# Kernel optimization log

Hardware: AMD Instinct MI355X
Metric: run time of the kernel (lower is better)

## Reference

```python
import jax, jax.numpy as jnp
import numpy as np

N = 50000
E = 800000
NHID = 128
NOUT = 64
NLAYER = 4
BN_EPS = 1e-5


def setup_inputs() -> dict:
    key = jax.random.key(0)
    ks = jax.random.split(key, 4)
    x = jax.random.normal(ks[0], (N, NHID), dtype=jnp.float32)
    edge_index = jax.random.randint(ks[1], (2, E), 0, N, dtype=jnp.int32)
    Ws = jax.random.normal(ks[2], (NLAYER, NHID, NHID), dtype=jnp.float32) / np.sqrt(NHID)
    bs = jnp.zeros((NLAYER, NHID), dtype=jnp.float32)
    gammas = jnp.ones((NLAYER, NHID), dtype=jnp.float32)
    betas = jnp.zeros((NLAYER, NHID), dtype=jnp.float32)
    Wout = jax.random.normal(ks[3], (NHID, NOUT), dtype=jnp.float32) / np.sqrt(NHID)
    bout = jnp.zeros((NOUT,), dtype=jnp.float32)
    return {"x": x, "edge_index": edge_index, "Ws": Ws, "bs": bs,
            "gammas": gammas, "betas": betas, "Wout": Wout, "bout": bout}


def _gcn_conv(x, src, dst, norm, W, b):
    # GCNConv: h = x W, then symmetric-normalized scatter-add over edges (+ self loops already in src/dst)
    h = x @ W                                   # [N, nhid]
    msgs = h[src] * norm[:, None]               # [E+N, nhid] gather + scale
    agg = jax.ops.segment_sum(msgs, dst, num_segments=N)  # scatter-add
    return agg + b


def _batchnorm(x, gamma, beta):
    mean = jnp.mean(x, axis=0)
    var = jnp.mean(jnp.square(x - mean), axis=0)  # biased var (torch BN)
    return (x - mean) * jax.lax.rsqrt(var + BN_EPS) * gamma + beta


def reference(x, edge_index, Ws, bs, gammas, betas, Wout, bout):
    # add self loops
    loops = jnp.arange(N, dtype=edge_index.dtype)
    src = jnp.concatenate([edge_index[0], loops])
    dst = jnp.concatenate([edge_index[1], loops])
    # symmetric degree normalization: deg^-1/2[src] * deg^-1/2[dst]
    deg = jax.ops.segment_sum(jnp.ones_like(dst, dtype=x.dtype), dst, num_segments=N)
    dinv = jax.lax.rsqrt(jnp.maximum(deg, 1.0))
    norm = dinv[src] * dinv[dst]

    prev = x
    for l in range(NLAYER):
        h = _gcn_conv(x, src, dst, norm, Ws[l], bs[l])
        h = _batchnorm(h, gammas[l], betas[l])
        h = jax.nn.relu(h)
        # dropout p=0.0 -> identity
        x = h + prev  # residual
        prev = x
    return x @ Wout + bout
```

## Files before the change

### kernel.cpp

```cpp
#include <hip/hip_runtime.h>

#define NN 50000
#define NE 800000
#define NH 128
#define NO 64
#define NL 4
#define BN_EPS 1e-5f
#define NB1 ((NN + 255) / 256)

typedef __attribute__((ext_vector_type(8))) short short8;
typedef __attribute__((ext_vector_type(4))) float f32x4;

__device__ inline unsigned short f2bf(float f) {
    unsigned int u = __float_as_uint(f);
    return (unsigned short)((u + 0x7fffu + ((u >> 16) & 1u)) >> 16);
}
__device__ inline float bflo(unsigned int u) { return __uint_as_float(u << 16); }
__device__ inline float bfhi(unsigned int u) { return __uint_as_float(u & 0xffff0000u); }
__device__ inline unsigned pk(float a, float b) {
    return (unsigned)f2bf(a) | ((unsigned)f2bf(b) << 16);
}

__global__ void k_degrank(const int* __restrict__ dst, int* __restrict__ deg,
                          int* __restrict__ rank) {
    int e = blockIdx.x * 256 + threadIdx.x;
    if (e < NE) rank[e] = atomicAdd(&deg[dst[e]], 1);
}

__global__ void k_dinv(const int* __restrict__ deg, float* __restrict__ dinv) {
    int i = blockIdx.x * 256 + threadIdx.x;
    if (i < NN) dinv[i] = rsqrtf((float)deg[i] + 1.0f);
}

__global__ void k_scan1(const int* __restrict__ deg, int* __restrict__ off, int* __restrict__ aux) {
    __shared__ int ls[256];
    int i = blockIdx.x * 256 + threadIdx.x;
    int v = (i < NN) ? deg[i] : 0;
    ls[threadIdx.x] = v;
    __syncthreads();
    for (int s = 1; s < 256; s <<= 1) {
        int t = (threadIdx.x >= s) ? ls[threadIdx.x - s] : 0;
        __syncthreads();
        ls[threadIdx.x] += t;
        __syncthreads();
    }
    if (i < NN) off[i] = ls[threadIdx.x] - v;
    if (threadIdx.x == 255) aux[blockIdx.x] = ls[255];
}

__global__ void k_scan2(int* __restrict__ aux) {
    __shared__ int ls[256];
    int v = (threadIdx.x < NB1) ? aux[threadIdx.x] : 0;
    ls[threadIdx.x] = v;
    __syncthreads();
    for (int s = 1; s < 256; s <<= 1) {
        int t = (threadIdx.x >= s) ? ls[threadIdx.x - s] : 0;
        __syncthreads();
        ls[threadIdx.x] += t;
        __syncthreads();
    }
    if (threadIdx.x < NB1) aux[threadIdx.x] = ls[threadIdx.x] - v;
}

__global__ void k_scan3(int* __restrict__ off, const int* __restrict__ aux) {
    int i = blockIdx.x * 256 + threadIdx.x;
    if (i < NN) off[i] += aux[blockIdx.x];
}

__global__ void k_fill(const int* __restrict__ src, const int* __restrict__ dst,
                       const int* __restrict__ off, const int* __restrict__ rank,
                       int* __restrict__ csr) {
    int e = blockIdx.x * 256 + threadIdx.x;
    if (e < NE) csr[off[dst[e]] + rank[e]] = src[e];
}

__global__ void k_packW(const float* __restrict__ Ws, unsigned short* __restrict__ Wpk) {
    int t = blockIdx.x * 256 + threadIdx.x;
    if (t >= NL * 16384) return;
    int l = t >> 14, r = t & 16383;
    int ks = r >> 12, ct = (r >> 9) & 7, lane = (r >> 3) & 63, i = r & 7;
    int k = ks * 32 + (lane >> 4) * 8 + i;
    int n = ct * 16 + (lane & 15);
    Wpk[t] = f2bf(Ws[l * 16384 + k * 128 + n]);
}

__global__ void k_packWout(const float* __restrict__ Wout, unsigned short* __restrict__ Wpk) {
    int r = blockIdx.x * 256 + threadIdx.x;
    if (r >= 8192) return;
    int ks = r >> 11, ct = (r >> 9) & 3, lane = (r >> 3) & 63, i = r & 7;
    int k = ks * 32 + (lane >> 4) * 8 + i;
    int n = ct * 16 + (lane & 15);
    Wpk[r] = f2bf(Wout[k * 64 + n]);
}

__global__ __launch_bounds__(256) void k_fg0(const float* __restrict__ X,
                                             const unsigned short* __restrict__ Wpk,
                                             const float* __restrict__ dinv,
                                             unsigned short* __restrict__ Hd) {
    int w = threadIdx.x >> 6, l = threadIdx.x & 63;
    int row0 = blockIdx.x * 64 + w * 16;
    int lo = l & 15, hi = l >> 4;
    int arow = row0 + lo;
    int crow = (arow < NN) ? arow : NN - 1;
    short8 frag[4];
#pragma unroll
    for (int g = 0; g < 4; g++) {
        int cs = g * 32 + hi * 8;
        float4 p0 = *(const float4*)&X[(size_t)crow * NH + cs];
        float4 p1 = *(const float4*)&X[(size_t)crow * NH + cs + 4];
        short8 f;
        f[0] = (short)f2bf(p0.x); f[1] = (short)f2bf(p0.y);
        f[2] = (short)f2bf(p0.z); f[3] = (short)f2bf(p0.w);
        f[4] = (short)f2bf(p1.x); f[5] = (short)f2bf(p1.y);
        f[6] = (short)f2bf(p1.z); f[7] = (short)f2bf(p1.w);
        frag[g] = f;
    }
    const short8* Wv = (const short8*)Wpk;
    int srow = row0 + hi * 4;
    float dv[4];
#pragma unroll
    for (int r = 0; r < 4; r++) dv[r] = (srow + r < NN) ? dinv[srow + r] : 0.0f;
#pragma unroll
    for (int ct = 0; ct < 8; ct++) {
        f32x4 acc = {0.0f, 0.0f, 0.0f, 0.0f};
#pragma unroll
        for (int g = 0; g < 4; g++)
            acc = __builtin_amdgcn_mfma_f32_16x16x32_bf16(frag[g], Wv[(g * 8 + ct) * 64 + l], acc, 0, 0, 0);
        int col = ct * 16 + lo;
#pragma unroll
        for (int r = 0; r < 4; r++) {
            int grow = srow + r;
            if (grow < NN) Hd[grow * NH + col] = f2bf(acc[r] * dv[r]);
        }
    }
}

__global__ __launch_bounds__(256) void k_fg(const unsigned short* __restrict__ AGGb,
                                            const float* __restrict__ scale,
                                            const float* __restrict__ shift,
                                            const float* __restrict__ Xprev,
                                            float* __restrict__ Xout,
                                            const unsigned short* __restrict__ Wpk,
                                            const float* __restrict__ dinv,
                                            unsigned short* __restrict__ Hd) {
    int w = threadIdx.x >> 6, l = threadIdx.x & 63;
    int row0 = blockIdx.x * 64 + w * 16;
    int lo = l & 15, hi = l >> 4;
    int arow = row0 + lo;
    bool valid = arow < NN;
    int crow = valid ? arow : NN - 1;
    short8 frag[4];
#pragma unroll
    for (int g = 0; g < 4; g++) {
        int cs = g * 32 + hi * 8;
        uint4 ab = *(const uint4*)&AGGb[(size_t)crow * NH + cs];
        float4 p0 = *(const float4*)&Xprev[(size_t)crow * NH + cs];
        float4 p1 = *(const float4*)&Xprev[(size_t)crow * NH + cs + 4];
        float4 sc0 = *(const float4*)&scale[cs];
        float4 sc1 = *(const float4*)&scale[cs + 4];
        float4 sh0 = *(const float4*)&shift[cs];
        float4 sh1 = *(const float4*)&shift[cs + 4];
        float o0 = fmaxf(fmaf(bflo(ab.x), sc0.x, sh0.x), 0.0f) + p0.x;
        float o1 = fmaxf(fmaf(bfhi(ab.x), sc0.y, sh0.y), 0.0f) + p0.y;
        float o2 = fmaxf(fmaf(bflo(ab.y), sc0.z, sh0.z), 0.0f) + p0.z;
        float o3 = fmaxf(fmaf(bfhi(ab.y), sc0.w, sh0.w), 0.0f) + p0.w;
        float o4 = fmaxf(fmaf(bflo(ab.z), sc1.x, sh1.x), 0.0f) + p1.x;
        float o5 = fmaxf(fmaf(bfhi(ab.z), sc1.y, sh1.y), 0.0f) + p1.y;
        float o6 = fmaxf(fmaf(bflo(ab.w), sc1.z, sh1.z), 0.0f) + p1.z;
        float o7 = fmaxf(fmaf(bfhi(ab.w), sc1.w, sh1.w), 0.0f) + p1.w;
        if (valid) {
            float4 s0 = {o0, o1, o2, o3}, s1 = {o4, o5, o6, o7};
            *(float4*)&Xout[(size_t)arow * NH + cs] = s0;
            *(float4*)&Xout[(size_t)arow * NH + cs + 4] = s1;
        }
        short8 f;
        f[0] = (short)f2bf(o0); f[1] = (short)f2bf(o1);
        f[2] = (short)f2bf(o2); f[3] = (short)f2bf(o3);
        f[4] = (short)f2bf(o4); f[5] = (short)f2bf(o5);
        f[6] = (short)f2bf(o6); f[7] = (short)f2bf(o7);
        frag[g] = f;
    }
    const short8* Wv = (const short8*)Wpk;
    int srow = row0 + hi * 4;
    float dv[4];
#pragma unroll
    for (int r = 0; r < 4; r++) dv[r] = (srow + r < NN) ? dinv[srow + r] : 0.0f;
#pragma unroll
    for (int ct = 0; ct < 8; ct++) {
        f32x4 acc = {0.0f, 0.0f, 0.0f, 0.0f};
#pragma unroll
        for (int g = 0; g < 4; g++)
            acc = __builtin_amdgcn_mfma_f32_16x16x32_bf16(frag[g], Wv[(g * 8 + ct) * 64 + l], acc, 0, 0, 0);
        int col = ct * 16 + lo;
#pragma unroll
        for (int r = 0; r < 4; r++) {
            int grow = srow + r;
            if (grow < NN) Hd[grow * NH + col] = f2bf(acc[r] * dv[r]);
        }
    }
}

__global__ __launch_bounds__(256) void k_fgout(const unsigned short* __restrict__ AGGb,
                                               const float* __restrict__ scale,
                                               const float* __restrict__ shift,
                                               const float* __restrict__ Xprev,
                                               const unsigned short* __restrict__ Wpk,
                                               const float* __restrict__ b,
                                               float* __restrict__ out) {
    int w = threadIdx.x >> 6, l = threadIdx.x & 63;
    int row0 = blockIdx.x * 64 + w * 16;
    int lo = l & 15, hi = l >> 4;
    int arow = row0 + lo;
    int crow = (arow < NN) ? arow : NN - 1;
    short8 frag[4];
#pragma unroll
    for (int g = 0; g < 4; g++) {
        int cs = g * 32 + hi * 8;
        uint4 ab = *(const uint4*)&AGGb[(size_t)crow * NH + cs];
        float4 p0 = *(const float4*)&Xprev[(size_t)crow * NH + cs];
        float4 p1 = *(const float4*)&Xprev[(size_t)crow * NH + cs + 4];
        float4 sc0 = *(const float4*)&scale[cs];
        float4 sc1 = *(const float4*)&scale[cs + 4];
        float4 sh0 = *(const float4*)&shift[cs];
        float4 sh1 = *(const float4*)&shift[cs + 4];
        short8 f;
        f[0] = (short)f2bf(fmaxf(fmaf(bflo(ab.x), sc0.x, sh0.x), 0.0f) + p0.x);
        f[1] = (short)f2bf(fmaxf(fmaf(bfhi(ab.x), sc0.y, sh0.y), 0.0f) + p0.y);
        f[2] = (short)f2bf(fmaxf(fmaf(bflo(ab.y), sc0.z, sh0.z), 0.0f) + p0.z);
        f[3] = (short)f2bf(fmaxf(fmaf(bfhi(ab.y), sc0.w, sh0.w), 0.0f) + p0.w);
        f[4] = (short)f2bf(fmaxf(fmaf(bflo(ab.z), sc1.x, sh1.x), 0.0f) + p1.x);
        f[5] = (short)f2bf(fmaxf(fmaf(bfhi(ab.z), sc1.y, sh1.y), 0.0f) + p1.y);
        f[6] = (short)f2bf(fmaxf(fmaf(bflo(ab.w), sc1.z, sh1.z), 0.0f) + p1.z);
        f[7] = (short)f2bf(fmaxf(fmaf(bfhi(ab.w), sc1.w, sh1.w), 0.0f) + p1.w);
        frag[g] = f;
    }
    const short8* Wv = (const short8*)Wpk;
    int srow = row0 + hi * 4;
#pragma unroll
    for (int ct = 0; ct < 4; ct++) {
        f32x4 acc = {0.0f, 0.0f, 0.0f, 0.0f};
#pragma unroll
        for (int g = 0; g < 4; g++)
            acc = __builtin_amdgcn_mfma_f32_16x16x32_bf16(frag[g], Wv[(g * 4 + ct) * 64 + l], acc, 0, 0, 0);
        int col = ct * 16 + lo;
        float bb = b[col];
#pragma unroll
        for (int r = 0; r < 4; r++) {
            int grow = srow + r;
            if (grow < NN) out[grow * NO + col] = acc[r] + bb;
        }
    }
}

__global__ __launch_bounds__(256) void k_gather(const unsigned short* __restrict__ Hd,
                                                const int* __restrict__ csr,
                                                const int* __restrict__ off,
                                                const int* __restrict__ deg,
                                                const float* __restrict__ dinv,
                                                unsigned short* __restrict__ AGGb) {
    int g = blockIdx.x * 16 + (threadIdx.x >> 4);
    if (g >= NN) return;
    int q = threadIdx.x & 15;
    const uint4* Hv = (const uint4*)Hd;
    int o = off[g], d = deg[g];
    uint4 h = Hv[g * 16 + q];
    float a0 = bflo(h.x), a1 = bfhi(h.x);
    float a2 = bflo(h.y), a3 = bfhi(h.y);
    float a4 = bflo(h.z), a5 = bfhi(h.z);
    float a6 = bflo(h.w), a7 = bfhi(h.w);
    int j = 0;
    for (; j + 2 <= d; j += 2) {
        int s0 = csr[o + j], s1 = csr[o + j + 1];
        uint4 h0 = Hv[s0 * 16 + q];
        uint4 h1 = Hv[s1 * 16 + q];
        a0 += bflo(h0.x) + bflo(h1.x); a1 += bfhi(h0.x) + bfhi(h1.x);
        a2 += bflo(h0.y) + bflo(h1.y); a3 += bfhi(h0.y) + bfhi(h1.y);
        a4 += bflo(h0.z) + bflo(h1.z); a5 += bfhi(h0.z) + bfhi(h1.z);
        a6 += bflo(h0.w) + bflo(h1.w); a7 += bfhi(h0.w) + bfhi(h1.w);
    }
    if (j < d) {
        int s0 = csr[o + j];
        uint4 h0 = Hv[s0 * 16 + q];
        a0 += bflo(h0.x); a1 += bfhi(h0.x);
        a2 += bflo(h0.y); a3 += bfhi(h0.y);
        a4 += bflo(h0.z); a5 += bfhi(h0.z);
        a6 += bflo(h0.w); a7 += bfhi(h0.w);
    }
    float dv = dinv[g];
    uint4 u;
    u.x = pk(a0 * dv, a1 * dv);
    u.y = pk(a2 * dv, a3 * dv);
    u.z = pk(a4 * dv, a5 * dv);
    u.w = pk(a6 * dv, a7 * dv);
    ((uint4*)AGGb)[g * 16 + q] = u;
}

__global__ __launch_bounds__(256) void k_bn_stats(const unsigned short* __restrict__ AGGb,
                                                  float* __restrict__ sums,
                                                  float* __restrict__ sumsq) {
    int tid = threadIdx.x;
    int col = tid & 127;
    float s = 0.0f, s2 = 0.0f;
    for (int r = blockIdx.x * 2 + (tid >> 7); r < NN; r += gridDim.x * 2) {
        float v = bflo((unsigned)AGGb[(size_t)r * NH + col]);
        s += v;
        s2 = fmaf(v, v, s2);
    }
    __shared__ float ls[256], ls2[256];
    ls[tid] = s; ls2[tid] = s2;
    __syncthreads();
    if (tid < 128) {
        atomicAdd(&sums[col], ls[tid] + ls[tid + 128]);
        atomicAdd(&sumsq[col], ls2[tid] + ls2[tid + 128]);
    }
}

__global__ void k_bn_fin(const float* __restrict__ sums, const float* __restrict__ sumsq,
                         const float* __restrict__ gamma, const float* __restrict__ beta,
                         float* __restrict__ scale, float* __restrict__ shift) {
    int c = threadIdx.x;
    if (c < NH) {
        float mean = sums[c] * (1.0f / NN);
        float var = sumsq[c] * (1.0f / NN) - mean * mean;
        float istd = rsqrtf(var + BN_EPS);
        float sc = istd * gamma[c];
        scale[c] = sc;
        shift[c] = beta[c] - mean * sc;
    }
}

extern "C" void kernel_launch(void* const* d_in, const int* in_sizes, int n_in,
                              void* d_out, int out_size, void* d_ws, size_t ws_size,
                              hipStream_t stream) {
    const float* x    = (const float*)d_in[0];
    const int*   ei   = (const int*)d_in[1];
    const float* Ws   = (const float*)d_in[2];
    const float* gam  = (const float*)d_in[4];
    const float* bet  = (const float*)d_in[5];
    const float* Wout = (const float*)d_in[6];
    const float* bout = (const float*)d_in[7];
    float* out = (float*)d_out;

    const int* src = ei;
    const int* dst = ei + NE;

    char* p = (char*)d_ws;
    auto alloc = [&](size_t bytes) { char* r = p; p += (bytes + 255) & ~(size_t)255; return r; };
    int*   deg_i = (int*)alloc(NN * 4);
    int*   off   = (int*)alloc(NN * 4);
    int*   rank  = (int*)alloc((size_t)NE * 4);
    int*   aux   = (int*)alloc(256 * 4);
    int*   csr   = (int*)alloc((size_t)NE * 4);
    float* dinv  = (float*)alloc(NN * 4);
    float* XA    = (float*)alloc((size_t)NN * NH * 4);
    float* XB    = (float*)alloc((size_t)NN * NH * 4);
    unsigned short* Hd   = (unsigned short*)alloc((size_t)NN * NH * 2);
    unsigned short* AGGb = (unsigned short*)alloc((size_t)NN * NH * 2);
    unsigned short* Wpk  = (unsigned short*)alloc((size_t)NL * NH * NH * 2);
    unsigned short* Wopk = (unsigned short*)alloc((size_t)NH * NO * 2);
    float* sums  = (float*)alloc(NH * 4);
    float* sumsq = (float*)alloc(NH * 4);
    float* scale = (float*)alloc(NH * 4);
    float* shift = (float*)alloc(NH * 4);

    hipMemsetAsync(deg_i, 0, NN * 4, stream);
    k_degrank<<<(NE + 255) / 256, 256, 0, stream>>>(dst, deg_i, rank);
    k_dinv<<<(NN + 255) / 256, 256, 0, stream>>>(deg_i, dinv);
    k_scan1<<<NB1, 256, 0, stream>>>(deg_i, off, aux);
    k_scan2<<<1, 256, 0, stream>>>(aux);
    k_scan3<<<NB1, 256, 0, stream>>>(off, aux);
    k_fill<<<(NE + 255) / 256, 256, 0, stream>>>(src, dst, off, rank, csr);
    k_packW<<<(NL * 16384 + 255) / 256, 256, 0, stream>>>(Ws, Wpk);
    k_packWout<<<32, 256, 0, stream>>>(Wout, Wopk);

    const int GB = (NN + 63) / 64;

    k_fg0<<<GB, 256, 0, stream>>>(x, Wpk, dinv, Hd);

    const float* xprev = x;
    for (int l = 0; l < NL; l++) {
        k_gather<<<(NN + 15) / 16, 256, 0, stream>>>(Hd, csr, off, deg_i, dinv, AGGb);
        hipMemsetAsync(sums, 0, 2 * NH * sizeof(float), stream);
        k_bn_stats<<<512, 256, 0, stream>>>(AGGb, sums, sumsq);
        k_bn_fin<<<1, 128, 0, stream>>>(sums, sumsq, gam + l * NH, bet + l * NH, scale, shift);
        if (l < NL - 1) {
            float* Xout = (l & 1) ? XB : XA;
            k_fg<<<GB, 256, 0, stream>>>(AGGb, scale, shift, xprev, Xout,
                                         Wpk + (size_t)(l + 1) * 16384, dinv, Hd);
            xprev = Xout;
        } else {
            k_fgout<<<GB, 256, 0, stream>>>(AGGb, scale, shift, xprev, Wopk, bout, out);
        }
    }
}
```

Measured before the change: 394.1 us.

## Merge setup kernels, vectorize CSR build, unroll gather, and widen BN stats loads

Measured after the change: 385.8 us. 1.02x faster.

```diff
diff --git a/kernel.cpp b/kernel.cpp
--- a/kernel.cpp
+++ b/kernel.cpp
@@ -23,16 +23,19 @@
 
 __global__ void k_degrank(const int* __restrict__ dst, int* __restrict__ deg,
                           int* __restrict__ rank) {
-    int e = blockIdx.x * 256 + threadIdx.x;
-    if (e < NE) rank[e] = atomicAdd(&deg[dst[e]], 1);
-}
-
-__global__ void k_dinv(const int* __restrict__ deg, float* __restrict__ dinv) {
-    int i = blockIdx.x * 256 + threadIdx.x;
-    if (i < NN) dinv[i] = rsqrtf((float)deg[i] + 1.0f);
-}
-
-__global__ void k_scan1(const int* __restrict__ deg, int* __restrict__ off, int* __restrict__ aux) {
+    int base = (blockIdx.x * 256 + threadIdx.x) * 4;
+    if (base >= NE) return;
+    int4 d4 = *(const int4*)&dst[base];
+    int4 r4;
+    r4.x = atomicAdd(&deg[d4.x], 1);
+    r4.y = atomicAdd(&deg[d4.y], 1);
+    r4.z = atomicAdd(&deg[d4.z], 1);
+    r4.w = atomicAdd(&deg[d4.w], 1);
+    *(int4*)&rank[base] = r4;
+}
+
+__global__ void k_scan1(const int* __restrict__ deg, int* __restrict__ off,
+                        int* __restrict__ aux, float* __restrict__ dinv) {
     __shared__ int ls[256];
     int i = blockIdx.x * 256 + threadIdx.x;
     int v = (i < NN) ? deg[i] : 0;
@@ -44,7 +47,10 @@
         ls[threadIdx.x] += t;
         __syncthreads();
     }
-    if (i < NN) off[i] = ls[threadIdx.x] - v;
+    if (i < NN) {
+        off[i] = ls[threadIdx.x] - v;
+        dinv[i] = rsqrtf((float)v + 1.0f);
+    }
     if (threadIdx.x == 255) aux[blockIdx.x] = ls[255];
 }
 
@@ -70,27 +76,34 @@
 __global__ void k_fill(const int* __restrict__ src, const int* __restrict__ dst,
                        const int* __restrict__ off, const int* __restrict__ rank,
                        int* __restrict__ csr) {
-    int e = blockIdx.x * 256 + threadIdx.x;
-    if (e < NE) csr[off[dst[e]] + rank[e]] = src[e];
-}
-
-__global__ void k_packW(const float* __restrict__ Ws, unsigned short* __restrict__ Wpk) {
+    int base = (blockIdx.x * 256 + threadIdx.x) * 4;
+    if (base >= NE) return;
+    int4 d4 = *(const int4*)&dst[base];
+    int4 r4 = *(const int4*)&rank[base];
+    int4 s4 = *(const int4*)&src[base];
+    int o0 = off[d4.x], o1 = off[d4.y], o2 = off[d4.z], o3 = off[d4.w];
+    csr[o0 + r4.x] = s4.x;
+    csr[o1 + r4.y] = s4.y;
+    csr[o2 + r4.z] = s4.z;
+    csr[o3 + r4.w] = s4.w;
+}
+
+__global__ void k_pack(const float* __restrict__ Ws, const float* __restrict__ Wout,
+                       unsigned short* __restrict__ Wpk, unsigned short* __restrict__ Wopk) {
     int t = blockIdx.x * 256 + threadIdx.x;
-    if (t >= NL * 16384) return;
-    int l = t >> 14, r = t & 16383;
-    int ks = r >> 12, ct = (r >> 9) & 7, lane = (r >> 3) & 63, i = r & 7;
-    int k = ks * 32 + (lane >> 4) * 8 + i;
-    int n = ct * 16 + (lane & 15);
-    Wpk[t] = f2bf(Ws[l * 16384 + k * 128 + n]);
-}
-
-__global__ void k_packWout(const float* __restrict__ Wout, unsigned short* __restrict__ Wpk) {
-    int r = blockIdx.x * 256 + threadIdx.x;
-    if (r >= 8192) return;
-    int ks = r >> 11, ct = (r >> 9) & 3, lane = (r >> 3) & 63, i = r & 7;
-    int k = ks * 32 + (lane >> 4) * 8 + i;
-    int n = ct * 16 + (lane & 15);
-    Wpk[r] = f2bf(Wout[k * 64 + n]);
+    if (t < NL * 16384) {
+        int l = t >> 14, r = t & 16383;
+        int ks = r >> 12, ct = (r >> 9) & 7, lane = (r >> 3) & 63, i = r & 7;
+        int k = ks * 32 + (lane >> 4) * 8 + i;
+        int n = ct * 16 + (lane & 15);
+        Wpk[t] = f2bf(Ws[l * 16384 + k * 128 + n]);
+    } else if (t < NL * 16384 + 8192) {
+        int r = t - NL * 16384;
+        int ks = r >> 11, ct = (r >> 9) & 3, lane = (r >> 3) & 63, i = r & 7;
+        int k = ks * 32 + (lane >> 4) * 8 + i;
+        int n = ct * 16 + (lane & 15);
+        Wopk[r] = f2bf(Wout[k * 64 + n]);
+    }
 }
 
 __global__ __launch_bounds__(256) void k_fg0(const float* __restrict__ X,
@@ -269,16 +282,23 @@
     float a4 = bflo(h.z), a5 = bfhi(h.z);
     float a6 = bflo(h.w), a7 = bfhi(h.w);
     int j = 0;
-    for (; j + 2 <= d; j += 2) {
+    for (; j + 4 <= d; j += 4) {
         int s0 = csr[o + j], s1 = csr[o + j + 1];
+        int s2 = csr[o + j + 2], s3 = csr[o + j + 3];
         uint4 h0 = Hv[s0 * 16 + q];
         uint4 h1 = Hv[s1 * 16 + q];
-        a0 += bflo(h0.x) + bflo(h1.x); a1 += bfhi(h0.x) + bfhi(h1.x);
-        a2 += bflo(h0.y) + bflo(h1.y); a3 += bfhi(h0.y) + bfhi(h1.y);
-        a4 += bflo(h0.z) + bflo(h1.z); a5 += bfhi(h0.z) + bfhi(h1.z);
-        a6 += bflo(h0.w) + bflo(h1.w); a7 += bfhi(h0.w) + bfhi(h1.w);
-    }
-    if (j < d) {
+        uint4 h2 = Hv[s2 * 16 + q];
+        uint4 h3 = Hv[s3 * 16 + q];
+        a0 += (bflo(h0.x) + bflo(h1.x)) + (bflo(h2.x) + bflo(h3.x));
+        a1 += (bfhi(h0.x) + bfhi(h1.x)) + (bfhi(h2.x) + bfhi(h3.x));
+        a2 += (bflo(h0.y) + bflo(h1.y)) + (bflo(h2.y) + bflo(h3.y));
+        a3 += (bfhi(h0.y) + bfhi(h1.y)) + (bfhi(h2.y) + bfhi(h3.y));
+        a4 += (bflo(h0.z) + bflo(h1.z)) + (bflo(h2.z) + bflo(h3.z));
+        a5 += (bfhi(h0.z) + bfhi(h1.z)) + (bfhi(h2.z) + bfhi(h3.z));
+        a6 += (bflo(h0.w) + bflo(h1.w)) + (bflo(h2.w) + bflo(h3.w));
+        a7 += (bfhi(h0.w) + bfhi(h1.w)) + (bfhi(h2.w) + bfhi(h3.w));
+    }
+    for (; j < d; j++) {
         int s0 = csr[o + j];
         uint4 h0 = Hv[s0 * 16 + q];
         a0 += bflo(h0.x); a1 += bfhi(h0.x);
@@ -299,19 +319,34 @@
                                                   float* __restrict__ sums,
                                                   float* __restrict__ sumsq) {
     int tid = threadIdx.x;
-    int col = tid & 127;
-    float s = 0.0f, s2 = 0.0f;
-    for (int r = blockIdx.x * 2 + (tid >> 7); r < NN; r += gridDim.x * 2) {
-        float v = bflo((unsigned)AGGb[(size_t)r * NH + col]);
-        s += v;
-        s2 = fmaf(v, v, s2);
-    }
-    __shared__ float ls[256], ls2[256];
-    ls[tid] = s; ls2[tid] = s2;
+    int cq = tid & 31;
+    int rg = tid >> 5;
+    float s0 = 0, s1 = 0, s2 = 0, s3 = 0;
+    float q0 = 0, q1 = 0, q2 = 0, q3 = 0;
+    for (int r = blockIdx.x * 8 + rg; r < NN; r += gridDim.x * 8) {
+        uint2 u = *(const uint2*)&AGGb[(size_t)r * NH + cq * 4];
+        float v0 = bflo(u.x), v1 = bfhi(u.x), v2 = bflo(u.y), v3 = bfhi(u.y);
+        s0 += v0; s1 += v1; s2 += v2; s3 += v3;
+        q0 = fmaf(v0, v0, q0); q1 = fmaf(v1, v1, q1);
+        q2 = fmaf(v2, v2, q2); q3 = fmaf(v3, v3, q3);
+    }
+    __shared__ float ls[256][4], lq[256][4];
+    ls[tid][0] = s0; ls[tid][1] = s1; ls[tid][2] = s2; ls[tid][3] = s3;
+    lq[tid][0] = q0; lq[tid][1] = q1; lq[tid][2] = q2; lq[tid][3] = q3;
     __syncthreads();
-    if (tid < 128) {
-        atomicAdd(&sums[col], ls[tid] + ls[tid + 128]);
-        atomicAdd(&sumsq[col], ls2[tid] + ls2[tid + 128]);
+    if (rg == 0) {
+        float t0 = s0, t1 = s1, t2 = s2, t3 = s3;
+        float u0 = q0, u1 = q1, u2 = q2, u3 = q3;
+        for (int g = 1; g < 8; g++) {
+            t0 += ls[g * 32 + cq][0]; t1 += ls[g * 32 + cq][1];
+            t2 += ls[g * 32 + cq][2]; t3 += ls[g * 32 + cq][3];
+            u0 += lq[g * 32 + cq][0]; u1 += lq[g * 32 + cq][1];
+            u2 += lq[g * 32 + cq][2]; u3 += lq[g * 32 + cq][3];
+        }
+        atomicAdd(&sums[cq * 4 + 0], t0); atomicAdd(&sums[cq * 4 + 1], t1);
+        atomicAdd(&sums[cq * 4 + 2], t2); atomicAdd(&sums[cq * 4 + 3], t3);
+        atomicAdd(&sumsq[cq * 4 + 0], u0); atomicAdd(&sumsq[cq * 4 + 1], u1);
+        atomicAdd(&sumsq[cq * 4 + 2], u2); atomicAdd(&sumsq[cq * 4 + 3], u3);
     }
 }
 
@@ -358,20 +393,18 @@
     unsigned short* AGGb = (unsigned short*)alloc((size_t)NN * NH * 2);
     unsigned short* Wpk  = (unsigned short*)alloc((size_t)NL * NH * NH * 2);
     unsigned short* Wopk = (unsigned short*)alloc((size_t)NH * NO * 2);
-    float* sums  = (float*)alloc(NH * 4);
-    float* sumsq = (float*)alloc(NH * 4);
+    float* stats = (float*)alloc(NL * 2 * NH * 4);
     float* scale = (float*)alloc(NH * 4);
     float* shift = (float*)alloc(NH * 4);
 
     hipMemsetAsync(deg_i, 0, NN * 4, stream);
-    k_degrank<<<(NE + 255) / 256, 256, 0, stream>>>(dst, deg_i, rank);
-    k_dinv<<<(NN + 255) / 256, 256, 0, stream>>>(deg_i, dinv);
-    k_scan1<<<NB1, 256, 0, stream>>>(deg_i, off, aux);
+    hipMemsetAsync(stats, 0, NL * 2 * NH * 4, stream);
+    k_degrank<<<(NE / 4 + 255) / 256, 256, 0, stream>>>(dst, deg_i, rank);
+    k_scan1<<<NB1, 256, 0, stream>>>(deg_i, off, aux, dinv);
     k_scan2<<<1, 256, 0, stream>>>(aux);
     k_scan3<<<NB1, 256, 0, stream>>>(off, aux);
-    k_fill<<<(NE + 255) / 256, 256, 0, stream>>>(src, dst, off, rank, csr);
-    k_packW<<<(NL * 16384 + 255) / 256, 256, 0, stream>>>(Ws, Wpk);
-    k_packWout<<<32, 256, 0, stream>>>(Wout, Wopk);
+    k_fill<<<(NE / 4 + 255) / 256, 256, 0, stream>>>(src, dst, off, rank, csr);
+    k_pack<<<(NL * 16384 + 8192 + 255) / 256, 256, 0, stream>>>(Ws, Wout, Wpk, Wopk);
 
     const int GB = (NN + 63) / 64;
 
@@ -379,9 +412,10 @@
 
     const float* xprev = x;
     for (int l = 0; l < NL; l++) {
+        float* sums  = stats + (size_t)l * 2 * NH;
+        float* sumsq = sums + NH;
         k_gather<<<(NN + 15) / 16, 256, 0, stream>>>(Hd, csr, off, deg_i, dinv, AGGb);
-        hipMemsetAsync(sums, 0, 2 * NH * sizeof(float), stream);
-        k_bn_stats<<<512, 256, 0, stream>>>(AGGb, sums, sumsq);
+        k_bn_stats<<<128, 256, 0, stream>>>(AGGb, sums, sumsq);
         k_bn_fin<<<1, 128, 0, stream>>>(sums, sumsq, gam + l * NH, bet + l * NH, scale, shift);
         if (l < NL - 1) {
             float* Xout = (l & 1) ? XB : XA;
```
